# Kernel tuning notes

Measured on AMD Instinct MI355X. Metric: run time of the kernel, lower is better.

The kernel has to match this reference:

```python
import jax, jax.numpy as jnp
import numpy as np

WINDOW = (8, 8)
NUM_HEADS = 6
PAD_H, PAD_W = WINDOW[0] // 2, WINDOW[1] // 2


def window_partition(x, wh, ww):
    # x: (B, C, H, W) -> (B*nh*nw, wh*ww, C)
    B, C, H, W = x.shape
    nh, nw = H // wh, W // ww
    x = x.reshape(B, C, nh, wh, nw, ww)
    x = x.transpose(0, 2, 4, 3, 5, 1)  # B, nh, nw, wh, ww, C
    return x.reshape(B * nh * nw, wh * ww, C)


def window_merge(x, B, C, H, W, wh, ww):
    # x: (B*nh*nw, wh*ww, C) -> (B, C, H, W)
    nh, nw = H // wh, W // ww
    x = x.reshape(B, nh, nw, wh, ww, C)
    x = x.transpose(0, 5, 1, 3, 2, 4)  # B, C, nh, wh, nw, ww
    return x.reshape(B, C, H, W)


def window_mha(t, num_heads):
    # t: (Bn, N, 3*C) packed qkv -> (Bn, N, C)
    Bn, N, C3 = t.shape
    C = C3 // 3
    d = C // num_heads
    q, k, v = jnp.split(t, 3, axis=-1)
    to_heads = lambda u: u.reshape(Bn, N, num_heads, d).transpose(0, 2, 1, 3)
    q, k, v = to_heads(q), to_heads(k), to_heads(v)
    scale = 1.0 / np.sqrt(d)
    attn = jax.nn.softmax(jnp.einsum('bhnd,bhmd->bhnm', q, k) * scale, axis=-1)
    o = jnp.einsum('bhnm,bhmd->bhnd', attn, v)
    return o.transpose(0, 2, 1, 3).reshape(Bn, N, C)


def setup_inputs() -> dict:
    key = jax.random.key(0)
    ks = jax.random.split(key, 5)
    B, C, H, W = 4, 384, 128, 128
    Cq = 64 * NUM_HEADS  # qkv_dim * num_heads = 384
    return {
        'x': jax.random.normal(ks[0], (B, C, H, W), dtype=jnp.float32),
        'w_qkv': jax.random.normal(ks[1], (3 * Cq, C), dtype=jnp.float32) * 0.02,
        'b_qkv': jax.random.normal(ks[2], (3 * Cq,), dtype=jnp.float32) * 0.02,
        'w_head': jax.random.normal(ks[3], (C, Cq), dtype=jnp.float32) * 0.02,
        'b_head': jax.random.normal(ks[4], (C,), dtype=jnp.float32) * 0.02,
    }


def reference(x, w_qkv, b_qkv, w_head, b_head):
    B, C, H, W = x.shape
    wh, ww = WINDOW
    # 1x1 conv qkv projection
    qkv = jnp.einsum('bchw,oc->bohw', x, w_qkv) + b_qkv[None, :, None, None]
    Cq = qkv.shape[1] // 3
    # branch 1: unpadded windows
    x1 = window_partition(qkv, wh, ww)
    x1 = window_mha(x1, NUM_HEADS)
    x1 = window_merge(x1, B, Cq, H, W, wh, ww)
    # branch 2: pad by half window, windows, then crop back
    qkv_p = jnp.pad(qkv, ((0, 0), (0, 0), (PAD_H, PAD_H), (PAD_W, PAD_W)))
    Hp, Wp = H + 2 * PAD_H, W + 2 * PAD_W
    x2 = window_partition(qkv_p, wh, ww)
    x2 = window_mha(x2, NUM_HEADS)
    x2 = window_merge(x2, B, Cq, Hp, Wp, wh, ww)
    x2 = x2[:, :, PAD_H:Hp - PAD_H, PAD_W:Wp - PAD_W]
    # merge + 1x1 conv head projection
    out = jnp.einsum('bchw,oc->bohw', x1 + x2, w_head) + b_head[None, :, None, None]
    return out
```

## Files before the change

### kernel.cpp

```cpp
#include <hip/hip_runtime.h>

typedef __bf16 bf16x8 __attribute__((ext_vector_type(8)));
typedef float f32x4 __attribute__((ext_vector_type(4)));

#define HW 16384
#define SP 66

union U4B8 { uint4 u; bf16x8 v; __bf16 h[8]; };
union U2B4 { uint2 u; __bf16 h[4]; };

__device__ __forceinline__ void gload_lds16(const __bf16* g, __bf16* l) {
    __builtin_amdgcn_global_load_lds(
        (const __attribute__((address_space(1))) unsigned int*)g,
        (__attribute__((address_space(3))) unsigned int*)l, 16, 0, 0);
}

__global__ __launch_bounds__(256) void k_prep(const float* __restrict__ x,
    __bf16* __restrict__ xT, const float* __restrict__ wq,
    __bf16* __restrict__ wqb)
{
    __shared__ __bf16 T[64 * 68];
    const int tid = threadIdx.x;
    const int bid = blockIdx.x;
    if (bid < 6144) {
        const int hw0 = (bid & 255) * 64;
        const int c0  = ((bid >> 8) % 6) * 64;
        const int b   = bid / 1536;
        const float* xb = x + (size_t)b * 384 * HW;
#pragma unroll
        for (int it = 0; it < 4; ++it) {
            int unit = it * 256 + tid;
            int c = unit >> 4, q = unit & 15;
            float4 f = *(const float4*)(xb + (size_t)(c0 + c) * HW + hw0 + q * 4);
            U2B4 t;
            t.h[0] = (__bf16)f.x; t.h[1] = (__bf16)f.y;
            t.h[2] = (__bf16)f.z; t.h[3] = (__bf16)f.w;
            *(uint2*)(T + c * 68 + q * 4) = t.u;
        }
        __syncthreads();
        __bf16* xtb = xT + (size_t)b * HW * 384;
#pragma unroll
        for (int it = 0; it < 2; ++it) {
            int unit = it * 256 + tid;
            int hw = unit >> 3, c8 = unit & 7;
            U4B8 t;
#pragma unroll
            for (int j = 0; j < 8; ++j) t.h[j] = T[(c8 * 8 + j) * 68 + hw];
            *(uint4*)(xtb + (size_t)(hw0 + hw) * 384 + c0 + c8 * 8) = t.u;
        }
    } else {
        int idx = ((bid - 6144) * 256 + tid) * 8;
        float4 f0 = *(const float4*)(wq + idx);
        float4 f1 = *(const float4*)(wq + idx + 4);
        U4B8 t;
        t.h[0] = (__bf16)f0.x; t.h[1] = (__bf16)f0.y;
        t.h[2] = (__bf16)f0.z; t.h[3] = (__bf16)f0.w;
        t.h[4] = (__bf16)f1.x; t.h[5] = (__bf16)f1.y;
        t.h[6] = (__bf16)f1.z; t.h[7] = (__bf16)f1.w;
        *(uint4*)(wqb + idx) = t.u;
    }
}

__global__ __launch_bounds__(256) void k_cvt(const float* __restrict__ src,
    __bf16* __restrict__ dst)
{
    int idx = (blockIdx.x * 256 + threadIdx.x) * 8;
    float4 f0 = *(const float4*)(src + idx);
    float4 f1 = *(const float4*)(src + idx + 4);
    U4B8 t;
    t.h[0] = (__bf16)f0.x; t.h[1] = (__bf16)f0.y;
    t.h[2] = (__bf16)f0.z; t.h[3] = (__bf16)f0.w;
    t.h[4] = (__bf16)f1.x; t.h[5] = (__bf16)f1.y;
    t.h[6] = (__bf16)f1.z; t.h[7] = (__bf16)f1.w;
    *(uint4*)(dst + idx) = t.u;
}

__global__ __launch_bounds__(256) void k_qkv(const __bf16* __restrict__ xT,
    const __bf16* __restrict__ wqb, const float* __restrict__ bq,
    __bf16* __restrict__ qk, __bf16* __restrict__ vT)
{
    __shared__ __bf16 As[2][128 * 32];
    __shared__ __bf16 Bs[2][128 * 32];
    const int tid = threadIdx.x;
    const int phys = blockIdx.x;
    const int logical = (phys & 7) * 576 + (phys >> 3);
    const int o0  = (logical % 9) * 128;
    const int rest = logical / 9;
    const int hw0 = (rest & 127) * 128;
    const int b   = rest >> 7;

    f32x4 acc[4][4];
#pragma unroll
    for (int i = 0; i < 4; ++i)
#pragma unroll
        for (int j = 0; j < 4; ++j)
#pragma unroll
            for (int e = 0; e < 4; ++e) acc[i][j][e] = 0.0f;

    const int l = tid & 63;
    const int wv = tid >> 6;
    const int wm = wv & 1;
    const int wn = wv >> 1;
    const int l16 = l & 15, quad = l >> 4;

    const __bf16* wrow = wqb + (size_t)o0 * 384;
    const __bf16* xrow = xT + (size_t)b * HW * 384 + (size_t)hw0 * 384;
    const int r = tid >> 2, c8 = (tid & 3) * 8;

    auto STAGE = [&](int buf, int kt) {
        const int c0 = kt * 32;
#pragma unroll
        for (int it = 0; it < 2; ++it) {
            int unit = it * 256 + tid;
            int rr = r + it * 64;
            gload_lds16(wrow + (size_t)rr * 384 + c0 + c8, &As[buf][unit * 8]);
            gload_lds16(xrow + (size_t)rr * 384 + c0 + c8, &Bs[buf][unit * 8]);
        }
    };

    STAGE(0, 0);
    __syncthreads();
    int cur = 0;
    for (int kt = 0; kt < 12; ++kt) {
        if (kt < 11) STAGE(cur ^ 1, kt + 1);
        bf16x8 a[4], bb[4];
#pragma unroll
        for (int t = 0; t < 4; ++t)
            a[t] = *(const bf16x8*)(&As[cur][(wm * 64 + t * 16 + l16) * 32 + quad * 8]);
#pragma unroll
        for (int t = 0; t < 4; ++t)
            bb[t] = *(const bf16x8*)(&Bs[cur][(wn * 64 + t * 16 + l16) * 32 + quad * 8]);
        __builtin_amdgcn_s_setprio(1);
#pragma unroll
        for (int mt = 0; mt < 4; ++mt)
#pragma unroll
            for (int nt = 0; nt < 4; ++nt)
                acc[mt][nt] = __builtin_amdgcn_mfma_f32_16x16x32_bf16(
                    a[mt], bb[nt], acc[mt][nt], 0, 0, 0);
        __builtin_amdgcn_s_setprio(0);
        if (kt < 11) __syncthreads();
        cur ^= 1;
    }

    if (o0 < 768) {
        __bf16* qb = qk + (size_t)b * HW * 768;
#pragma unroll
        for (int mt = 0; mt < 4; ++mt) {
            int oo = o0 + wm * 64 + mt * 16 + quad * 4;
            float4 bias = *(const float4*)(bq + oo);
#pragma unroll
            for (int nt = 0; nt < 4; ++nt) {
                int hw = hw0 + wn * 64 + nt * 16 + l16;
                U2B4 t;
                t.h[0] = (__bf16)(acc[mt][nt][0] + bias.x);
                t.h[1] = (__bf16)(acc[mt][nt][1] + bias.y);
                t.h[2] = (__bf16)(acc[mt][nt][2] + bias.z);
                t.h[3] = (__bf16)(acc[mt][nt][3] + bias.w);
                *(uint2*)(qb + (size_t)hw * 768 + oo) = t.u;
            }
        }
    } else {
        __bf16* vb = vT + (size_t)b * 384 * HW;
#pragma unroll
        for (int mt = 0; mt < 4; ++mt) {
            int oo = o0 + wm * 64 + mt * 16 + quad * 4;
            float4 bias = *(const float4*)(bq + oo);
            int vo = oo - 768;
#pragma unroll
            for (int nt = 0; nt < 4; ++nt) {
                int hw = hw0 + wn * 64 + nt * 16 + l16;
                vb[(size_t)(vo + 0) * HW + hw] = (__bf16)(acc[mt][nt][0] + bias.x);
                vb[(size_t)(vo + 1) * HW + hw] = (__bf16)(acc[mt][nt][1] + bias.y);
                vb[(size_t)(vo + 2) * HW + hw] = (__bf16)(acc[mt][nt][2] + bias.z);
                vb[(size_t)(vo + 3) * HW + hw] = (__bf16)(acc[mt][nt][3] + bias.w);
            }
        }
    }
}

__global__ __launch_bounds__(192) void k_attn1(const __bf16* __restrict__ qk,
    const __bf16* __restrict__ vT, __bf16* __restrict__ y1)
{
    __shared__ __bf16 sm[3][64 * SP];
    const int tid = threadIdx.x;
    const int l = tid & 63, wv = tid >> 6;
    const int wid = blockIdx.x * 3 + wv;
    const int head = wid % 6;
    const int win = wid / 6;
    const int wx = win & 15;
    const int wy = (win >> 4) & 15;
    const int b  = win >> 8;
    const int h0 = wy * 8, w0 = wx * 8;
    const __bf16* qb = qk + (size_t)b * HW * 768;
    const __bf16* vb = vT + (size_t)b * 384 * HW;
    __bf16* P = &sm[wv][0];
    const int l16 = l & 15, quad = l >> 4;
    const int cbase = head * 64;

    U4B8 vreg[2][4];
#pragma unroll
    for (int ks = 0; ks < 2; ++ks) {
        const int hh2 = h0 + ks * 4 + quad;
#pragma unroll
        for (int t = 0; t < 4; ++t)
            vreg[ks][t].u = *(const uint4*)(vb +
                (size_t)(cbase + t * 16 + l16) * HW + (hh2 * 128 + w0));
    }

    size_t toff[4];
#pragma unroll
    for (int t = 0; t < 4; ++t) {
        int tok = t * 16 + l16;
        toff[t] = (size_t)((h0 + (tok >> 3)) * 128 + w0 + (tok & 7)) * 768;
    }

    f32x4 s[4][4];
#pragma unroll
    for (int i = 0; i < 4; ++i)
#pragma unroll
        for (int j = 0; j < 4; ++j)
#pragma unroll
            for (int e = 0; e < 4; ++e) s[i][j][e] = 0.0f;

#pragma unroll
    for (int ks = 0; ks < 2; ++ks) {
        bf16x8 aq[4], bk[4];
#pragma unroll
        for (int t = 0; t < 4; ++t) {
            U4B8 uq, uk;
            uq.u = *(const uint4*)(qb + toff[t] + cbase + ks * 32 + quad * 8);
            uk.u = *(const uint4*)(qb + toff[t] + 384 + cbase + ks * 32 + quad * 8);
            aq[t] = uq.v;
            bk[t] = uk.v;
        }
        __builtin_amdgcn_s_setprio(1);
#pragma unroll
        for (int mt = 0; mt < 4; ++mt)
#pragma unroll
            for (int nt = 0; nt < 4; ++nt)
                s[mt][nt] = __builtin_amdgcn_mfma_f32_16x16x32_bf16(
                    aq[mt], bk[nt], s[mt][nt], 0, 0, 0);
        __builtin_amdgcn_s_setprio(0);
    }

#pragma unroll
    for (int mt = 0; mt < 4; ++mt) {
#pragma unroll
        for (int e = 0; e < 4; ++e) {
            float p[4];
#pragma unroll
            for (int nt = 0; nt < 4; ++nt) p[nt] = __expf(s[mt][nt][e] * 0.125f);
            float sum = (p[0] + p[1]) + (p[2] + p[3]);
#pragma unroll
            for (int st = 1; st < 16; st <<= 1) sum += __shfl_xor(sum, st, 64);
            float r = __fdividef(1.0f, sum);
            int row = mt * 16 + quad * 4 + e;
#pragma unroll
            for (int nt = 0; nt < 4; ++nt)
                P[row * SP + nt * 16 + l16] = (__bf16)(p[nt] * r);
        }
    }

    f32x4 o[4][4];
#pragma unroll
    for (int i = 0; i < 4; ++i)
#pragma unroll
        for (int j = 0; j < 4; ++j)
#pragma unroll
            for (int e = 0; e < 4; ++e) o[i][j][e] = 0.0f;

#pragma unroll
    for (int ks = 0; ks < 2; ++ks) {
        bf16x8 ap[4];
#pragma unroll
        for (int t = 0; t < 4; ++t)
            ap[t] = *(const bf16x8*)(P + (t * 16 + l16) * SP + ks * 32 + quad * 8);
        __builtin_amdgcn_s_setprio(1);
#pragma unroll
        for (int mt = 0; mt < 4; ++mt)
#pragma unroll
            for (int nt = 0; nt < 4; ++nt)
                o[mt][nt] = __builtin_amdgcn_mfma_f32_16x16x32_bf16(
                    ap[mt], vreg[ks][nt].v, o[mt][nt], 0, 0, 0);
        __builtin_amdgcn_s_setprio(0);
    }

#pragma unroll
    for (int mt = 0; mt < 4; ++mt)
#pragma unroll
        for (int e = 0; e < 4; ++e) {
            int row = mt * 16 + quad * 4 + e;
#pragma unroll
            for (int nt = 0; nt < 4; ++nt)
                P[row * SP + nt * 16 + l16] = (__bf16)o[mt][nt][e];
        }

    __bf16* yb = y1 + (size_t)b * HW * 384;
#pragma unroll
    for (int it = 0; it < 8; ++it) {
        int unit = it * 64 + l;
        int tok = unit >> 3, c8 = unit & 7;
        int hh = h0 + (tok >> 3), ww = w0 + (tok & 7);
        *(uint4*)(yb + (size_t)(hh * 128 + ww) * 384 + cbase + c8 * 8) =
            *(const uint4*)(P + tok * SP + c8 * 8);
    }
}

__global__ __launch_bounds__(192) void k_attn2(const __bf16* __restrict__ qk,
    const __bf16* __restrict__ vT, const __bf16* __restrict__ y1,
    __bf16* __restrict__ ysum)
{
    __shared__ __bf16 sm[3][64 * SP];
    const int tid = threadIdx.x;
    const int l = tid & 63, wv = tid >> 6;
    const int wid = blockIdx.x * 3 + wv;
    const int head = wid % 6;
    const int win = wid / 6;
    const int wx = win % 17;
    const int t2 = win / 17;
    const int wy = t2 % 17;
    const int b  = t2 / 17;
    const int h0 = wy * 8 - 4;
    const int w0 = wx * 8 - 4;
    const __bf16* qb = qk + (size_t)b * HW * 768;
    const __bf16* vb = vT + (size_t)b * 384 * HW;
    __bf16* P = &sm[wv][0];
    const int l16 = l & 15, quad = l >> 4;
    const int cbase = head * 64;

    U4B8 vreg[2][4];
#pragma unroll
    for (int ks = 0; ks < 2; ++ks) {
        const int hh2 = h0 + ks * 4 + quad;
        const bool rowok = ((unsigned)hh2 < 128u);
#pragma unroll
        for (int t = 0; t < 4; ++t) {
            U4B8 u;
            u.u = make_uint4(0, 0, 0, 0);
            if (rowok) {
                const __bf16* vp = vb + (size_t)(cbase + t * 16 + l16) * HW
                                   + (hh2 * 128 + w0);
                if (w0 >= 0)   *(uint2*)&u.h[0] = *(const uint2*)vp;
                if (w0 <= 120) *(uint2*)&u.h[4] = *(const uint2*)(vp + 4);
            }
            vreg[ks][t] = u;
        }
    }

    size_t toff[4]; bool tval[4];
#pragma unroll
    for (int t = 0; t < 4; ++t) {
        int tok = t * 16 + l16;
        int hh = h0 + (tok >> 3), ww = w0 + (tok & 7);
        tval[t] = ((unsigned)hh < 128u && (unsigned)ww < 128u);
        toff[t] = tval[t] ? (size_t)(hh * 128 + ww) * 768 : 0;
    }

    f32x4 s[4][4];
#pragma unroll
    for (int i = 0; i < 4; ++i)
#pragma unroll
        for (int j = 0; j < 4; ++j)
#pragma unroll
            for (int e = 0; e < 4; ++e) s[i][j][e] = 0.0f;

#pragma unroll
    for (int ks = 0; ks < 2; ++ks) {
        bf16x8 aq[4], bk[4];
#pragma unroll
        for (int t = 0; t < 4; ++t) {
            U4B8 uq, uk;
            if (tval[t]) {
                uq.u = *(const uint4*)(qb + toff[t] + cbase + ks * 32 + quad * 8);
                uk.u = *(const uint4*)(qb + toff[t] + 384 + cbase + ks * 32 + quad * 8);
            } else {
                uq.u = make_uint4(0, 0, 0, 0);
                uk.u = make_uint4(0, 0, 0, 0);
            }
            aq[t] = uq.v;
            bk[t] = uk.v;
        }
        __builtin_amdgcn_s_setprio(1);
#pragma unroll
        for (int mt = 0; mt < 4; ++mt)
#pragma unroll
            for (int nt = 0; nt < 4; ++nt)
                s[mt][nt] = __builtin_amdgcn_mfma_f32_16x16x32_bf16(
                    aq[mt], bk[nt], s[mt][nt], 0, 0, 0);
        __builtin_amdgcn_s_setprio(0);
    }

#pragma unroll
    for (int mt = 0; mt < 4; ++mt) {
#pragma unroll
        for (int e = 0; e < 4; ++e) {
            float p[4];
#pragma unroll
            for (int nt = 0; nt < 4; ++nt) p[nt] = __expf(s[mt][nt][e] * 0.125f);
            float sum = (p[0] + p[1]) + (p[2] + p[3]);
#pragma unroll
            for (int st = 1; st < 16; st <<= 1) sum += __shfl_xor(sum, st, 64);
            float r = __fdividef(1.0f, sum);
            int row = mt * 16 + quad * 4 + e;
#pragma unroll
            for (int nt = 0; nt < 4; ++nt)
                P[row * SP + nt * 16 + l16] = (__bf16)(p[nt] * r);
        }
    }

    f32x4 o[4][4];
#pragma unroll
    for (int i = 0; i < 4; ++i)
#pragma unroll
        for (int j = 0; j < 4; ++j)
#pragma unroll
            for (int e = 0; e < 4; ++e) o[i][j][e] = 0.0f;

#pragma unroll
    for (int ks = 0; ks < 2; ++ks) {
        bf16x8 ap[4];
#pragma unroll
        for (int t = 0; t < 4; ++t)
            ap[t] = *(const bf16x8*)(P + (t * 16 + l16) * SP + ks * 32 + quad * 8);
        __builtin_amdgcn_s_setprio(1);
#pragma unroll
        for (int mt = 0; mt < 4; ++mt)
#pragma unroll
            for (int nt = 0; nt < 4; ++nt)
                o[mt][nt] = __builtin_amdgcn_mfma_f32_16x16x32_bf16(
                    ap[mt], vreg[ks][nt].v, o[mt][nt], 0, 0, 0);
        __builtin_amdgcn_s_setprio(0);
    }

#pragma unroll
    for (int mt = 0; mt < 4; ++mt)
#pragma unroll
        for (int e = 0; e < 4; ++e) {
            int row = mt * 16 + quad * 4 + e;
#pragma unroll
            for (int nt = 0; nt < 4; ++nt)
                P[row * SP + nt * 16 + l16] = (__bf16)o[mt][nt][e];
        }

    const __bf16* y1b = y1 + (size_t)b * HW * 384;
    __bf16* yb = ysum + (size_t)b * HW * 384;
#pragma unroll
    for (int it = 0; it < 8; ++it) {
        int unit = it * 64 + l;
        int tok = unit >> 3, c8 = unit & 7;
        int hh = h0 + (tok >> 3), ww = w0 + (tok & 7);
        if ((unsigned)hh < 128u && (unsigned)ww < 128u) {
            size_t off = (size_t)(hh * 128 + ww) * 384 + cbase + c8 * 8;
            U4B8 t1, t2, r;
            t1.u = *(const uint4*)(y1b + off);
            t2.u = *(const uint4*)(P + tok * SP + c8 * 8);
#pragma unroll
            for (int e = 0; e < 8; ++e)
                r.h[e] = (__bf16)((float)t1.h[e] + (float)t2.h[e]);
            *(uint4*)(yb + off) = r.u;
        }
    }
}

__global__ __launch_bounds__(256) void k_head(const __bf16* __restrict__ ysum,
    const __bf16* __restrict__ whb, const float* __restrict__ bh,
    float* __restrict__ out)
{
    __shared__ __bf16 As[2][128 * 32];
    __shared__ __bf16 Bs[2][128 * 32];
    const int tid = threadIdx.x;
    const int phys = blockIdx.x;
    const int logical = (phys & 7) * 192 + (phys >> 3);
    const int o0  = (logical % 3) * 128;
    const int rest = logical / 3;
    const int hw0 = (rest & 127) * 128;
    const int b   = rest >> 7;

    f32x4 acc[4][4];
#pragma unroll
    for (int i = 0; i < 4; ++i)
#pragma unroll
        for (int j = 0; j < 4; ++j)
#pragma unroll
            for (int e = 0; e < 4; ++e) acc[i][j][e] = 0.0f;

    const int l = tid & 63, wv = tid >> 6;
    const int wm = wv & 1;
    const int wn = wv >> 1;
    const int l16 = l & 15, quad = l >> 4;

    const __bf16* yrow = ysum + (size_t)b * HW * 384 + (size_t)hw0 * 384;
    const __bf16* wrow = whb + (size_t)o0 * 384;
    const int r = tid >> 2, c8 = (tid & 3) * 8;

    auto STAGE = [&](int buf, int kt) {
        const int c0 = kt * 32;
#pragma unroll
        for (int it = 0; it < 2; ++it) {
            int unit = it * 256 + tid;
            int rr = r + it * 64;
            gload_lds16(yrow + (size_t)rr * 384 + c0 + c8, &As[buf][unit * 8]);
            gload_lds16(wrow + (size_t)rr * 384 + c0 + c8, &Bs[buf][unit * 8]);
        }
    };

    STAGE(0, 0);
    __syncthreads();
    int cur = 0;
    for (int kt = 0; kt < 12; ++kt) {
        if (kt < 11) STAGE(cur ^ 1, kt + 1);
        bf16x8 a[4], bb[4];
#pragma unroll
        for (int t = 0; t < 4; ++t)
            a[t] = *(const bf16x8*)(&As[cur][(wm * 64 + t * 16 + l16) * 32 + quad * 8]);
#pragma unroll
        for (int t = 0; t < 4; ++t)
            bb[t] = *(const bf16x8*)(&Bs[cur][(wn * 64 + t * 16 + l16) * 32 + quad * 8]);
        __builtin_amdgcn_s_setprio(1);
#pragma unroll
        for (int mt = 0; mt < 4; ++mt)
#pragma unroll
            for (int nt = 0; nt < 4; ++nt)
                acc[mt][nt] = __builtin_amdgcn_mfma_f32_16x16x32_bf16(
                    a[mt], bb[nt], acc[mt][nt], 0, 0, 0);
        __builtin_amdgcn_s_setprio(0);
        if (kt < 11) __syncthreads();
        cur ^= 1;
    }

#pragma unroll
    for (int nt = 0; nt < 4; ++nt) {
        int oo = o0 + wn * 64 + nt * 16 + l16;
        float bb_ = bh[oo];
        float* ob = out + ((size_t)b * 384 + oo) * HW + hw0 + wm * 64;
#pragma unroll
        for (int mt = 0; mt < 4; ++mt) {
            float4 f;
            f.x = acc[mt][nt][0] + bb_;
            f.y = acc[mt][nt][1] + bb_;
            f.z = acc[mt][nt][2] + bb_;
            f.w = acc[mt][nt][3] + bb_;
            *(float4*)(ob + mt * 16 + quad * 4) = f;
        }
    }
}

extern "C" void kernel_launch(void* const* d_in, const int* in_sizes, int n_in,
                              void* d_out, int out_size, void* d_ws, size_t ws_size,
                              hipStream_t stream) {
    const float* x  = (const float*)d_in[0];
    const float* wq = (const float*)d_in[1];
    const float* bq = (const float*)d_in[2];
    const float* wh = (const float*)d_in[3];
    const float* bh = (const float*)d_in[4];
    float* out = (float*)d_out;

    __bf16* qk = (__bf16*)d_ws;
    __bf16* vT = qk + (size_t)4 * HW * 768;
    __bf16* y1 = vT + (size_t)4 * 384 * HW;
    __bf16* ys = y1 + (size_t)4 * HW * 384;
    __bf16* xT   = y1;
    __bf16* wqb  = ys;
    __bf16* whb  = vT;

    k_prep <<<dim3(6360), 256, 0, stream>>>(x, xT, wq, wqb);
    k_qkv  <<<dim3(4608), 256, 0, stream>>>(xT, wqb, bq, qk, vT);
    k_attn1<<<dim3(2048), 192, 0, stream>>>(qk, vT, y1);
    k_attn2<<<dim3(2312), 192, 0, stream>>>(qk, vT, y1, ys);
    k_cvt  <<<dim3(72),   256, 0, stream>>>(wh, whb);
    k_head <<<dim3(1536), 256, 0, stream>>>(ys, whb, bh, out);
}
```

Baseline: 458.8 us.

## Triple-buffer LDS staging in QKV and head GEMMs with partial vmcnt waits

Both the QKV projection and head projection GEMMs move from a double-buffered to a triple-buffered LDS pipeline. Loads are issued two k-tiles ahead and only the oldest stage is waited on through explicit s_waitcnt vmcnt counts instead of a full __syncthreads drain. The aim is to keep more global-to-LDS loads in flight and hide memory latency behind the MFMA work. The cost is 50% more LDS per block, which may reduce occupancy, plus hand-counted vmcnt values that depend on the compiler not reordering or adding other vector memory ops.

```diff
diff --git a/kernel.cpp b/kernel.cpp
--- a/kernel.cpp
+++ b/kernel.cpp
@@ -79,8 +79,8 @@
     const __bf16* __restrict__ wqb, const float* __restrict__ bq,
     __bf16* __restrict__ qk, __bf16* __restrict__ vT)
 {
-    __shared__ __bf16 As[2][128 * 32];
-    __shared__ __bf16 Bs[2][128 * 32];
+    __shared__ __bf16 As[3][128 * 32];
+    __shared__ __bf16 Bs[3][128 * 32];
     const int tid = threadIdx.x;
     const int phys = blockIdx.x;
     const int logical = (phys & 7) * 576 + (phys >> 3);
@@ -119,10 +119,19 @@
     };
 
     STAGE(0, 0);
-    __syncthreads();
-    int cur = 0;
+    STAGE(1, 1);
+#pragma unroll
     for (int kt = 0; kt < 12; ++kt) {
-        if (kt < 11) STAGE(cur ^ 1, kt + 1);
+        const int cur = kt % 3;
+        if (kt < 10) {
+            STAGE((kt + 2) % 3, kt + 2);
+            asm volatile("s_waitcnt vmcnt(8)" ::: "memory");
+        } else if (kt == 10) {
+            asm volatile("s_waitcnt vmcnt(4)" ::: "memory");
+        } else {
+            asm volatile("s_waitcnt vmcnt(0)" ::: "memory");
+        }
+        __builtin_amdgcn_s_barrier();
         bf16x8 a[4], bb[4];
 #pragma unroll
         for (int t = 0; t < 4; ++t)
@@ -138,8 +147,7 @@
                 acc[mt][nt] = __builtin_amdgcn_mfma_f32_16x16x32_bf16(
                     a[mt], bb[nt], acc[mt][nt], 0, 0, 0);
         __builtin_amdgcn_s_setprio(0);
-        if (kt < 11) __syncthreads();
-        cur ^= 1;
+        __builtin_amdgcn_s_barrier();
     }
 
     if (o0 < 768) {
@@ -466,8 +474,8 @@
     const __bf16* __restrict__ whb, const float* __restrict__ bh,
     float* __restrict__ out)
 {
-    __shared__ __bf16 As[2][128 * 32];
-    __shared__ __bf16 Bs[2][128 * 32];
+    __shared__ __bf16 As[3][128 * 32];
+    __shared__ __bf16 Bs[3][128 * 32];
     const int tid = threadIdx.x;
     const int phys = blockIdx.x;
     const int logical = (phys & 7) * 192 + (phys >> 3);
@@ -505,10 +513,19 @@
     };
 
     STAGE(0, 0);
-    __syncthreads();
-    int cur = 0;
+    STAGE(1, 1);
+#pragma unroll
     for (int kt = 0; kt < 12; ++kt) {
-        if (kt < 11) STAGE(cur ^ 1, kt + 1);
+        const int cur = kt % 3;
+        if (kt < 10) {
+            STAGE((kt + 2) % 3, kt + 2);
+            asm volatile("s_waitcnt vmcnt(8)" ::: "memory");
+        } else if (kt == 10) {
+            asm volatile("s_waitcnt vmcnt(4)" ::: "memory");
+        } else {
+            asm volatile("s_waitcnt vmcnt(0)" ::: "memory");
+        }
+        __builtin_amdgcn_s_barrier();
         bf16x8 a[4], bb[4];
 #pragma unroll
         for (int t = 0; t < 4; ++t)
@@ -524,8 +541,7 @@
                 acc[mt][nt] = __builtin_amdgcn_mfma_f32_16x16x32_bf16(
                     a[mt], bb[nt], acc[mt][nt], 0, 0, 0);
         __builtin_amdgcn_s_setprio(0);
-        if (kt < 11) __syncthreads();
-        cur ^= 1;
+        __builtin_amdgcn_s_barrier();
     }
 
 #pragma unroll
```

Result: no change. 454.9 us (-0.8%).
